# Kernel tuning notes

Measured on AMD Instinct MI355X. Metric: run time of the kernel, lower is better.

## Reference

```python
import jax, jax.numpy as jnp
import numpy as np

ATTN_WINDOW = 7  # attention_window from attn_params; dilation (attention_stride) = 1


def _xavier(key, shape):
    lim = np.sqrt(6.0 / (shape[0] + shape[1]))
    return jax.random.uniform(key, shape, jnp.float32, -lim, lim)


def setup_inputs() -> dict:
    key = jax.random.key(0)
    ks = jax.random.split(key, 8)
    B, Cin, Him, Wim = 4, 3, 112, 112
    Cmid, Cout = 128, 128
    x = jax.random.normal(ks[0], (B, Cin, Him, Wim), jnp.float32)
    conv_w = jax.random.normal(ks[1], (Cmid, Cin, 3, 3), jnp.float32) * 0.1  # OIHW
    conv_b = jnp.zeros((Cmid,), jnp.float32)
    q_w = _xavier(ks[2], (Cmid, Cmid)); q_b = jnp.zeros((Cmid,), jnp.float32)
    k_w = _xavier(ks[3], (Cmid, Cmid)); k_b = jnp.zeros((Cmid,), jnp.float32)
    v_w = _xavier(ks[4], (Cout, Cmid)); v_b = jnp.zeros((Cout,), jnp.float32)
    return {"x": x, "conv_w": conv_w, "conv_b": conv_b,
            "q_w": q_w, "q_b": q_b, "k_w": k_w, "k_b": k_b, "v_w": v_w, "v_b": v_b}


def _neighbor_idx(n, ksz):
    # NATTEN-style neighborhood: centered window, clamped to stay inside the image.
    starts = jnp.clip(jnp.arange(n) - ksz // 2, 0, n - ksz)
    return starts[:, None] + jnp.arange(ksz)[None, :]  # [n, ksz]


def reference(x, conv_w, conv_b, q_w, q_b, k_w, k_b, v_w, v_b):
    # conv stem (3x3, stride 2, pad 1) + ReLU
    f = jax.lax.conv_general_dilated(
        x, conv_w, window_strides=(2, 2), padding=[(1, 1), (1, 1)],
        dimension_numbers=("NCHW", "OIHW", "NCHW"))
    f = jax.nn.relu(f + conv_b[None, :, None, None])
    f = f.transpose(0, 2, 3, 1)  # NHWC  [B,H,W,Cmid]
    # 1x1 convs == per-pixel linear layers
    q = f @ q_w.T + q_b
    k = f @ k_w.T + k_b
    v = f @ v_w.T + v_b
    B, H, W, C = q.shape
    ksz = min(ATTN_WINDOW, H, W)
    ksz -= 1 if ksz % 2 == 0 else 0
    ih = _neighbor_idx(H, ksz)  # [H, ksz]
    iw = _neighbor_idx(W, ksz)  # [W, ksz]
    # gather per-pixel neighborhoods: [B,H,W,ksz,ksz,C]
    kn = k[:, ih[:, None, :, None], iw[None, :, None, :], :]
    vn = v[:, ih[:, None, :, None], iw[None, :, None, :], :]
    scale = C ** -0.5
    logits = jnp.einsum("bhwc,bhwijc->bhwij", q * scale, kn)
    attn = jax.nn.softmax(logits.reshape(B, H, W, -1), axis=-1).reshape(logits.shape)
    out = jnp.einsum("bhwij,bhwijc->bhwc", attn, vn)  # [B,H,W,Cout]
    return out.transpose(0, 3, 1, 2)  # back to NCHW
```

## Files before the change

kernel.cpp:

```cpp
#include <hip/hip_runtime.h>
#include <hip/hip_bf16.h>
#include <math.h>

#define HW 56
#define PPI (HW*HW)
#define NB 4
#define C 128
#define NPIX (NB*PPI)

typedef __attribute__((ext_vector_type(8))) short short8;
typedef __attribute__((ext_vector_type(4))) float f32x4;

__device__ __forceinline__ short bfbits(float v) {
    __hip_bfloat16 hb = __float2bfloat16(v);
    return *reinterpret_cast<short*>(&hb);
}

__global__ __launch_bounds__(256) void prep_kernel(
    const float* __restrict__ cw,
    const float* __restrict__ qw, const float* __restrict__ kw,
    const float* __restrict__ vw,
    __hip_bfloat16* __restrict__ wcf, __hip_bfloat16* __restrict__ wqkv)
{
    int gid = blockIdx.x * 256 + threadIdx.x;
    if (blockIdx.x < 192) {
        int m   = gid >> 14;
        int r   = gid & 16383;
        int col = r >> 7;
        int k   = r & 127;
        const float* W = (m == 0) ? qw : (m == 1) ? kw : vw;
        int kk = k >> 5, hi = (k >> 3) & 3, j = k & 7;
        wqkv[m * 16384 + ((kk * 4 + hi) * 128 + col) * 8 + j] = __float2bfloat16(W[col * 128 + k]);
    } else {
        int idx = gid - 192 * 256;
        int hi = idx >> 10, cout = (idx >> 3) & 127, j = idx & 7;
        int k  = hi * 8 + j;
        float v = (k < 27) ? cw[cout * 27 + k] : 0.f;
        wcf[(hi * 128 + cout) * 8 + j] = __float2bfloat16(v);
    }
}

__global__ __launch_bounds__(256) void convqkv_kernel(
    const float* __restrict__ x, const __hip_bfloat16* __restrict__ wcf,
    const float* __restrict__ cb, const __hip_bfloat16* __restrict__ wqkv,
    const float* __restrict__ qb, const float* __restrict__ kb,
    const float* __restrict__ vb,
    __hip_bfloat16* __restrict__ qo, __hip_bfloat16* __restrict__ ko,
    __hip_bfloat16* __restrict__ vo)
{
    __shared__ __align__(16) short f_lds[16 * 128];

    int t = threadIdx.x, lane = t & 63, wid = t >> 6;
    int r16 = lane & 15, hi = lane >> 4;

    int bx = blockIdx.x;
    int bimg = bx / 196;
    int rr = bx % 196;
    int th = rr / 14, tw = rr % 14;

    int h = th * 4 + (r16 >> 2), w = tw * 4 + (r16 & 3);
    short8 af;
    #pragma unroll
    for (int j = 0; j < 8; ++j) {
        int k = hi * 8 + j;
        float xv = 0.f;
        if (k < 27) {
            int ci = k / 9, r9 = k % 9;
            int kh = r9 / 3, kw_ = r9 % 3;
            int ih = 2 * h - 1 + kh, iw = 2 * w - 1 + kw_;
            if (ih >= 0 && ih < 112 && iw >= 0 && iw < 112)
                xv = x[((size_t)(bimg * 3 + ci) * 112 + ih) * 112 + iw];
        }
        af[j] = bfbits(xv);
    }

    #pragma unroll
    for (int ctl = 0; ctl < 2; ++ctl) {
        int ct = wid * 2 + ctl;
        int cout = ct * 16 + r16;
        short8 bw = *(const short8*)((const short*)wcf + (hi * 128 + cout) * 8);
        f32x4 acc = {0.f, 0.f, 0.f, 0.f};
        acc = __builtin_amdgcn_mfma_f32_16x16x32_bf16(af, bw, acc, 0, 0, 0);
        float bias = cb[cout];
        int colblk = cout >> 3, inb = (cout & 7) * 2;
        #pragma unroll
        for (int rg = 0; rg < 4; ++rg) {
            int px = hi * 4 + rg;
            float v = fmaxf(acc[rg] + bias, 0.f);
            *(short*)((char*)f_lds + px * 256 + ((colblk ^ px) << 4) + inb) = bfbits(v);
        }
    }
    __syncthreads();

    short8 fa[4];
    #pragma unroll
    for (int kk = 0; kk < 4; ++kk) {
        int colblk = kk * 4 + hi;
        fa[kk] = *(const short8*)((char*)f_lds + r16 * 256 + ((colblk ^ r16) << 4));
    }

    #pragma unroll
    for (int i = 0; i < 6; ++i) {
        int idx = wid * 6 + i;
        int mat = idx >> 3, nt = idx & 7;
        const short* wb = (const short*)wqkv + mat * 16384 + hi * 1024 + r16 * 8 + nt * 128;
        f32x4 acc = {0.f, 0.f, 0.f, 0.f};
        acc = __builtin_amdgcn_mfma_f32_16x16x32_bf16(fa[0], *(const short8*)(wb),         acc, 0, 0, 0);
        acc = __builtin_amdgcn_mfma_f32_16x16x32_bf16(fa[1], *(const short8*)(wb +  4096), acc, 0, 0, 0);
        acc = __builtin_amdgcn_mfma_f32_16x16x32_bf16(fa[2], *(const short8*)(wb +  8192), acc, 0, 0, 0);
        acc = __builtin_amdgcn_mfma_f32_16x16x32_bf16(fa[3], *(const short8*)(wb + 12288), acc, 0, 0, 0);
        int col = nt * 16 + r16;
        const float* Bv   = (mat == 0) ? qb : (mat == 1) ? kb : vb;
        __hip_bfloat16* O = (mat == 0) ? qo : (mat == 1) ? ko : vo;
        float bb = Bv[col];
        #pragma unroll
        for (int rg = 0; rg < 4; ++rg) {
            int px = hi * 4 + rg;
            int hh = th * 4 + (px >> 2), ww = tw * 4 + (px & 3);
            O[((size_t)(bimg * PPI + hh * HW + ww)) * C + col] = __float2bfloat16(acc[rg] + bb);
        }
    }
}

#define VPITCH 272

__global__ __launch_bounds__(256) void attn_kernel(
    const __hip_bfloat16* __restrict__ qg, const __hip_bfloat16* __restrict__ kg,
    const __hip_bfloat16* __restrict__ vg, float* __restrict__ out)
{
    __shared__ __align__(16) short vT[128 * 136];
    __shared__ __align__(16) float logit_s[16 * 116];
    __shared__ __align__(16) short attnW[16 * 136];

    int t    = threadIdx.x;
    int lane = t & 63, wid = t >> 6;
    int r16  = lane & 15, hi = lane >> 4;

    int bx = blockIdx.x;
    int b  = bx / 196;
    int rr = bx % 196;
    int th = rr / 14, tw = rr % 14;
    int ih0 = min(max(th*4 - 3, 0), HW - 10);
    int iw0 = min(max(tw*4 - 3, 0), HW - 10);

    {
        unsigned* aw = (unsigned*)attnW;
        for (int i = t; i < 1088; i += 256) aw[i] = 0u;
    }

    const unsigned* vgu = (const unsigned*)vg;
    #pragma unroll 4
    for (int it = 0; it < 16; ++it) {
        int i  = t + 256*it;
        int np = i >> 6;
        int c2 = i & 63;
        int n0 = min(2*np,     99);
        int n1 = min(2*np + 1, 99);
        int p0 = b*PPI + (ih0 + n0/10)*HW + (iw0 + n0%10);
        int p1 = b*PPI + (ih0 + n1/10)*HW + (iw0 + n1%10);
        unsigned av = vgu[(size_t)p0*64 + c2];
        unsigned bv = vgu[(size_t)p1*64 + c2];
        unsigned w0 = (av & 0xffffu) | (bv << 16);
        unsigned w1 = (av >> 16)     | (bv & 0xffff0000u);
        int c    = 2*c2;
        int hsw  = (c >> 3) & 7;
        int off  = (4*np) ^ (hsw << 4);
        *(unsigned*)((char*)vT + c*VPITCH + off)          = w0;
        *(unsigned*)((char*)vT + c*VPITCH + VPITCH + off) = w1;
    }

    int ph = th*4 + (r16 >> 2), pw = tw*4 + (r16 & 3);
    const short* qrow = (const short*)qg + (size_t)(b*PPI + ph*HW + pw)*C + hi*8;
    short8 qa0 = *(const short8*)(qrow);
    short8 qa1 = *(const short8*)(qrow + 32);
    short8 qa2 = *(const short8*)(qrow + 64);
    short8 qa3 = *(const short8*)(qrow + 96);

    __syncthreads();

    for (int nt = wid; nt < 7; nt += 4) {
        int n  = nt*16 + r16;
        int nc = min(n, 99);
        int kp = b*PPI + (ih0 + nc/10)*HW + (iw0 + nc%10);
        const short* krow = (const short*)kg + (size_t)kp*C + hi*8;
        f32x4 acc = {0.f, 0.f, 0.f, 0.f};
        acc = __builtin_amdgcn_mfma_f32_16x16x32_bf16(qa0, *(const short8*)(krow),      acc, 0, 0, 0);
        acc = __builtin_amdgcn_mfma_f32_16x16x32_bf16(qa1, *(const short8*)(krow + 32), acc, 0, 0, 0);
        acc = __builtin_amdgcn_mfma_f32_16x16x32_bf16(qa2, *(const short8*)(krow + 64), acc, 0, 0, 0);
        acc = __builtin_amdgcn_mfma_f32_16x16x32_bf16(qa3, *(const short8*)(krow + 96), acc, 0, 0, 0);
        #pragma unroll
        for (int rg = 0; rg < 4; ++rg)
            logit_s[(hi*4 + rg)*116 + nt*16 + r16] = acc[rg];
    }
    __syncthreads();

    {
        int r7 = lane / 7, s7 = lane - 7*r7;
        bool valid = lane < 49;
        const float scale = 0.08838834764831845f;
        #pragma unroll
        for (int px = 0; px < 4; ++px) {
            int p = wid*4 + px;
            int h = th*4 + (p >> 2), w = tw*4 + (p & 3);
            int hs = min(max(h - 3, 0), HW - 7);
            int ws = min(max(w - 3, 0), HW - 7);
            int col = (hs - ih0 + r7)*10 + (ws - iw0 + s7);
            float lg = valid ? logit_s[p*116 + col] * scale : -INFINITY;
            float m = lg;
            #pragma unroll
            for (int d = 1; d < 64; d <<= 1) m = fmaxf(m, __shfl_xor(m, d));
            float e = valid ? __expf(lg - m) : 0.f;
            float s = e;
            #pragma unroll
            for (int d = 1; d < 64; d <<= 1) s += __shfl_xor(s, d);
            if (valid) {
                __hip_bfloat16 hb = __float2bfloat16(e / s);
                *(__hip_bfloat16*)((char*)attnW + p*VPITCH + 2*col) = hb;
            }
        }
    }
    __syncthreads();

    short8 pa[4];
    #pragma unroll
    for (int kk = 0; kk < 4; ++kk)
        pa[kk] = *(const short8*)((char*)attnW + r16*VPITCH + kk*64 + hi*16);

    for (int nt = wid; nt < 8; nt += 4) {
        int c   = nt*16 + r16;
        int hsw = (c >> 3) & 7;
        const char* vrow = (const char*)vT + c*VPITCH;
        f32x4 acc = {0.f, 0.f, 0.f, 0.f};
        #pragma unroll
        for (int kk = 0; kk < 4; ++kk) {
            short8 vb = *(const short8*)(vrow + ((kk*64 + hi*16) ^ (hsw << 4)));
            acc = __builtin_amdgcn_mfma_f32_16x16x32_bf16(pa[kk], vb, acc, 0, 0, 0);
        }
        #pragma unroll
        for (int rg = 0; rg < 4; ++rg) {
            int p = hi*4 + rg;
            int h = th*4 + (p >> 2), w = tw*4 + (p & 3);
            out[(((size_t)b*C + c)*HW + h)*HW + w] = acc[rg];
        }
    }
}

extern "C" void kernel_launch(void* const* d_in, const int* in_sizes, int n_in,
                              void* d_out, int out_size, void* d_ws, size_t ws_size,
                              hipStream_t stream) {
    const float* x      = (const float*)d_in[0];
    const float* conv_w = (const float*)d_in[1];
    const float* conv_b = (const float*)d_in[2];
    const float* q_w    = (const float*)d_in[3];
    const float* q_b    = (const float*)d_in[4];
    const float* k_w    = (const float*)d_in[5];
    const float* k_b    = (const float*)d_in[6];
    const float* v_w    = (const float*)d_in[7];
    const float* v_b    = (const float*)d_in[8];
    float* out = (float*)d_out;

    __hip_bfloat16* q_bf  = (__hip_bfloat16*)d_ws;
    __hip_bfloat16* k_bf  = q_bf + (size_t)NPIX * C;
    __hip_bfloat16* v_bf  = k_bf + (size_t)NPIX * C;
    __hip_bfloat16* wqkv  = v_bf + (size_t)NPIX * C;
    __hip_bfloat16* wcf   = wqkv + 3 * 16384;

    prep_kernel<<<208, 256, 0, stream>>>(conv_w, q_w, k_w, v_w, wcf, wqkv);
    convqkv_kernel<<<NB*196, 256, 0, stream>>>(x, wcf, conv_b, wqkv,
                                               q_b, k_b, v_b, q_bf, k_bf, v_bf);
    attn_kernel<<<NB*196, 256, 0, stream>>>(q_bf, k_bf, v_bf, out);
}
```

Measured before the change: 44.44 us.

## Fuse conv stem, QKV projection and neighborhood attention into one kernel

Replaces the separate conv+QKV kernel and attention kernel with a single fused kernel. Each block recomputes the conv stem and K/V projections for its 10x10 neighborhood halo directly into LDS, and computes Q only for its own 16 pixels. This removes the bf16 Q/K/V workspace writes and reads and one launch, but redundantly recomputes halo features and raises LDS usage, which limits occupancy.

```diff
diff --git a/kernel.cpp b/kernel.cpp
--- a/kernel.cpp
+++ b/kernel.cpp
@@ -14,6 +14,9 @@
 __device__ __forceinline__ short bfbits(float v) {
     __hip_bfloat16 hb = __float2bfloat16(v);
     return *reinterpret_cast<short*>(&hb);
+}
+__device__ __forceinline__ unsigned packbf(float a, float b) {
+    return (unsigned)(unsigned short)bfbits(a) | ((unsigned)(unsigned short)bfbits(b) << 16);
 }
 
 __global__ __launch_bounds__(256) void prep_kernel(
@@ -40,101 +43,24 @@
     }
 }
 
-__global__ __launch_bounds__(256) void convqkv_kernel(
+#define VPITCH 272
+
+__global__ __launch_bounds__(256, 2) void fused_kernel(
     const float* __restrict__ x, const __hip_bfloat16* __restrict__ wcf,
     const float* __restrict__ cb, const __hip_bfloat16* __restrict__ wqkv,
     const float* __restrict__ qb, const float* __restrict__ kb,
-    const float* __restrict__ vb,
-    __hip_bfloat16* __restrict__ qo, __hip_bfloat16* __restrict__ ko,
-    __hip_bfloat16* __restrict__ vo)
+    const float* __restrict__ vb, float* __restrict__ out)
 {
-    __shared__ __align__(16) short f_lds[16 * 128];
+    __shared__ __align__(16) short k_lds[112 * 128];
+    __shared__ __align__(16) short vT[128 * 136];
+    __shared__ __align__(16) short q_lds[16 * 128];
+    __shared__ __align__(16) char  uni_s[16 * 116 * 4];
+    __shared__ __align__(16) short attnW[16 * 136];
+    short* f_ch    = (short*)uni_s;
+    float* logit_s = (float*)uni_s;
 
     int t = threadIdx.x, lane = t & 63, wid = t >> 6;
     int r16 = lane & 15, hi = lane >> 4;
-
-    int bx = blockIdx.x;
-    int bimg = bx / 196;
-    int rr = bx % 196;
-    int th = rr / 14, tw = rr % 14;
-
-    int h = th * 4 + (r16 >> 2), w = tw * 4 + (r16 & 3);
-    short8 af;
-    #pragma unroll
-    for (int j = 0; j < 8; ++j) {
-        int k = hi * 8 + j;
-        float xv = 0.f;
-        if (k < 27) {
-            int ci = k / 9, r9 = k % 9;
-            int kh = r9 / 3, kw_ = r9 % 3;
-            int ih = 2 * h - 1 + kh, iw = 2 * w - 1 + kw_;
-            if (ih >= 0 && ih < 112 && iw >= 0 && iw < 112)
-                xv = x[((size_t)(bimg * 3 + ci) * 112 + ih) * 112 + iw];
-        }
-        af[j] = bfbits(xv);
-    }
-
-    #pragma unroll
-    for (int ctl = 0; ctl < 2; ++ctl) {
-        int ct = wid * 2 + ctl;
-        int cout = ct * 16 + r16;
-        short8 bw = *(const short8*)((const short*)wcf + (hi * 128 + cout) * 8);
-        f32x4 acc = {0.f, 0.f, 0.f, 0.f};
-        acc = __builtin_amdgcn_mfma_f32_16x16x32_bf16(af, bw, acc, 0, 0, 0);
-        float bias = cb[cout];
-        int colblk = cout >> 3, inb = (cout & 7) * 2;
-        #pragma unroll
-        for (int rg = 0; rg < 4; ++rg) {
-            int px = hi * 4 + rg;
-            float v = fmaxf(acc[rg] + bias, 0.f);
-            *(short*)((char*)f_lds + px * 256 + ((colblk ^ px) << 4) + inb) = bfbits(v);
-        }
-    }
-    __syncthreads();
-
-    short8 fa[4];
-    #pragma unroll
-    for (int kk = 0; kk < 4; ++kk) {
-        int colblk = kk * 4 + hi;
-        fa[kk] = *(const short8*)((char*)f_lds + r16 * 256 + ((colblk ^ r16) << 4));
-    }
-
-    #pragma unroll
-    for (int i = 0; i < 6; ++i) {
-        int idx = wid * 6 + i;
-        int mat = idx >> 3, nt = idx & 7;
-        const short* wb = (const short*)wqkv + mat * 16384 + hi * 1024 + r16 * 8 + nt * 128;
-        f32x4 acc = {0.f, 0.f, 0.f, 0.f};
-        acc = __builtin_amdgcn_mfma_f32_16x16x32_bf16(fa[0], *(const short8*)(wb),         acc, 0, 0, 0);
-        acc = __builtin_amdgcn_mfma_f32_16x16x32_bf16(fa[1], *(const short8*)(wb +  4096), acc, 0, 0, 0);
-        acc = __builtin_amdgcn_mfma_f32_16x16x32_bf16(fa[2], *(const short8*)(wb +  8192), acc, 0, 0, 0);
-        acc = __builtin_amdgcn_mfma_f32_16x16x32_bf16(fa[3], *(const short8*)(wb + 12288), acc, 0, 0, 0);
-        int col = nt * 16 + r16;
-        const float* Bv   = (mat == 0) ? qb : (mat == 1) ? kb : vb;
-        __hip_bfloat16* O = (mat == 0) ? qo : (mat == 1) ? ko : vo;
-        float bb = Bv[col];
-        #pragma unroll
-        for (int rg = 0; rg < 4; ++rg) {
-            int px = hi * 4 + rg;
-            int hh = th * 4 + (px >> 2), ww = tw * 4 + (px & 3);
-            O[((size_t)(bimg * PPI + hh * HW + ww)) * C + col] = __float2bfloat16(acc[rg] + bb);
-        }
-    }
-}
-
-#define VPITCH 272
-
-__global__ __launch_bounds__(256) void attn_kernel(
-    const __hip_bfloat16* __restrict__ qg, const __hip_bfloat16* __restrict__ kg,
-    const __hip_bfloat16* __restrict__ vg, float* __restrict__ out)
-{
-    __shared__ __align__(16) short vT[128 * 136];
-    __shared__ __align__(16) float logit_s[16 * 116];
-    __shared__ __align__(16) short attnW[16 * 136];
-
-    int t    = threadIdx.x;
-    int lane = t & 63, wid = t >> 6;
-    int r16  = lane & 15, hi = lane >> 4;
 
     int bx = blockIdx.x;
     int b  = bx / 196;
@@ -146,48 +72,138 @@
     {
         unsigned* aw = (unsigned*)attnW;
         for (int i = t; i < 1088; i += 256) aw[i] = 0u;
-    }
-
-    const unsigned* vgu = (const unsigned*)vg;
-    #pragma unroll 4
-    for (int it = 0; it < 16; ++it) {
-        int i  = t + 256*it;
-        int np = i >> 6;
-        int c2 = i & 63;
-        int n0 = min(2*np,     99);
-        int n1 = min(2*np + 1, 99);
-        int p0 = b*PPI + (ih0 + n0/10)*HW + (iw0 + n0%10);
-        int p1 = b*PPI + (ih0 + n1/10)*HW + (iw0 + n1%10);
-        unsigned av = vgu[(size_t)p0*64 + c2];
-        unsigned bv = vgu[(size_t)p1*64 + c2];
-        unsigned w0 = (av & 0xffffu) | (bv << 16);
-        unsigned w1 = (av >> 16)     | (bv & 0xffff0000u);
-        int c    = 2*c2;
-        int hsw  = (c >> 3) & 7;
-        int off  = (4*np) ^ (hsw << 4);
-        *(unsigned*)((char*)vT + c*VPITCH + off)          = w0;
-        *(unsigned*)((char*)vT + c*VPITCH + VPITCH + off) = w1;
-    }
-
-    int ph = th*4 + (r16 >> 2), pw = tw*4 + (r16 & 3);
-    const short* qrow = (const short*)qg + (size_t)(b*PPI + ph*HW + pw)*C + hi*8;
-    short8 qa0 = *(const short8*)(qrow);
-    short8 qa1 = *(const short8*)(qrow + 32);
-    short8 qa2 = *(const short8*)(qrow + 64);
-    short8 qa3 = *(const short8*)(qrow + 96);
-
-    __syncthreads();
+        for (int i = t; i < 1024; i += 256) {
+            int c = i >> 3, j = i & 7;
+            int hsw = (c >> 3) & 7;
+            int unit = (14 + (j >> 2)) ^ hsw;
+            *(unsigned*)((char*)vT + c*VPITCH + (unit << 4) + (j & 3)*4) = 0u;
+        }
+    }
+
+    int cout0 = (wid*2 + 0)*16 + r16;
+    int cout1 = (wid*2 + 1)*16 + r16;
+    short8 cbw0 = *(const short8*)((const short*)wcf + (hi*128 + cout0)*8);
+    short8 cbw1 = *(const short8*)((const short*)wcf + (hi*128 + cout1)*8);
+
+    auto conv_to_fch = [&](int hf, int wf) {
+        short8 af;
+        #pragma unroll
+        for (int j = 0; j < 8; ++j) {
+            int k = hi*8 + j;
+            float xv = 0.f;
+            if (k < 27) {
+                int ci = k/9, r9 = k%9, kh = r9/3, kw_ = r9%3;
+                int ih = 2*hf - 1 + kh, iw = 2*wf - 1 + kw_;
+                if (ih >= 0 && ih < 112 && iw >= 0 && iw < 112)
+                    xv = x[((size_t)(b*3 + ci)*112 + ih)*112 + iw];
+            }
+            af[j] = bfbits(xv);
+        }
+        #pragma unroll
+        for (int ctl = 0; ctl < 2; ++ctl) {
+            int cout  = ctl ? cout1 : cout0;
+            short8 bw = ctl ? cbw1  : cbw0;
+            f32x4 acc = {0.f, 0.f, 0.f, 0.f};
+            acc = __builtin_amdgcn_mfma_f32_16x16x32_bf16(af, bw, acc, 0, 0, 0);
+            float bias = cb[cout];
+            int colblk = cout >> 3, inb = (cout & 7)*2;
+            #pragma unroll
+            for (int rg = 0; rg < 4; ++rg) {
+                int px = hi*4 + rg;
+                *(short*)((char*)f_ch + px*256 + ((colblk ^ px) << 4) + inb)
+                    = bfbits(fmaxf(acc[rg] + bias, 0.f));
+            }
+        }
+    };
+
+    for (int cc = 0; cc < 7; ++cc) {
+        int nc = min(cc*16 + r16, 99);
+        conv_to_fch(ih0 + nc/10, iw0 + nc%10);
+        __syncthreads();
+
+        short8 fa[4];
+        #pragma unroll
+        for (int kk = 0; kk < 4; ++kk)
+            fa[kk] = *(const short8*)((char*)f_ch + r16*256 + (((kk*4 + hi) ^ r16) << 4));
+
+        #pragma unroll
+        for (int i = 0; i < 4; ++i) {
+            int idx = wid*4 + i;
+            int mv  = idx >> 3;
+            int ct  = idx & 7;
+            const short* wb = (const short*)wqkv + (1+mv)*16384 + hi*1024 + r16*8 + ct*128;
+            f32x4 acc = {0.f, 0.f, 0.f, 0.f};
+            acc = __builtin_amdgcn_mfma_f32_16x16x32_bf16(fa[0], *(const short8*)(wb),         acc, 0, 0, 0);
+            acc = __builtin_amdgcn_mfma_f32_16x16x32_bf16(fa[1], *(const short8*)(wb +  4096), acc, 0, 0, 0);
+            acc = __builtin_amdgcn_mfma_f32_16x16x32_bf16(fa[2], *(const short8*)(wb +  8192), acc, 0, 0, 0);
+            acc = __builtin_amdgcn_mfma_f32_16x16x32_bf16(fa[3], *(const short8*)(wb + 12288), acc, 0, 0, 0);
+            int c = ct*16 + r16;
+            if (mv == 0) {
+                float bb = kb[c];
+                int swz = c >> 3;
+                #pragma unroll
+                for (int rg = 0; rg < 4; ++rg) {
+                    int n = cc*16 + hi*4 + rg;
+                    *(short*)((char*)k_lds + n*256 + ((swz ^ (n & 15)) << 4) + (c & 7)*2)
+                        = bfbits(acc[rg] + bb);
+                }
+            } else {
+                float bb = vb[c];
+                int n0 = cc*16 + hi*4;
+                unsigned lo  = packbf(acc[0] + bb, acc[1] + bb);
+                unsigned hi2 = packbf(acc[2] + bb, acc[3] + bb);
+                int hsw = (c >> 3) & 7;
+                int off = (2*n0) ^ (hsw << 4);
+                *(uint2*)((char*)vT + c*VPITCH + off) = make_uint2(lo, hi2);
+            }
+        }
+        __syncthreads();
+    }
+
+    {
+        int ph = th*4 + (r16 >> 2), pw = tw*4 + (r16 & 3);
+        conv_to_fch(ph, pw);
+        __syncthreads();
+
+        short8 fa[4];
+        #pragma unroll
+        for (int kk = 0; kk < 4; ++kk)
+            fa[kk] = *(const short8*)((char*)f_ch + r16*256 + (((kk*4 + hi) ^ r16) << 4));
+
+        #pragma unroll
+        for (int i = 0; i < 2; ++i) {
+            int ct = wid*2 + i;
+            const short* wb = (const short*)wqkv + hi*1024 + r16*8 + ct*128;
+            f32x4 acc = {0.f, 0.f, 0.f, 0.f};
+            acc = __builtin_amdgcn_mfma_f32_16x16x32_bf16(fa[0], *(const short8*)(wb),         acc, 0, 0, 0);
+            acc = __builtin_amdgcn_mfma_f32_16x16x32_bf16(fa[1], *(const short8*)(wb +  4096), acc, 0, 0, 0);
+            acc = __builtin_amdgcn_mfma_f32_16x16x32_bf16(fa[2], *(const short8*)(wb +  8192), acc, 0, 0, 0);
+            acc = __builtin_amdgcn_mfma_f32_16x16x32_bf16(fa[3], *(const short8*)(wb + 12288), acc, 0, 0, 0);
+            int c = ct*16 + r16;
+            float bb = qb[c];
+            #pragma unroll
+            for (int rg = 0; rg < 4; ++rg) {
+                int px = hi*4 + rg;
+                *(short*)((char*)q_lds + px*256 + (((c >> 3) ^ px) << 4) + (c & 7)*2)
+                    = bfbits(acc[rg] + bb);
+            }
+        }
+        __syncthreads();
+    }
+
+    short8 qa[4];
+    #pragma unroll
+    for (int kk = 0; kk < 4; ++kk)
+        qa[kk] = *(const short8*)((char*)q_lds + r16*256 + (((kk*4 + hi) ^ r16) << 4));
 
     for (int nt = wid; nt < 7; nt += 4) {
-        int n  = nt*16 + r16;
-        int nc = min(n, 99);
-        int kp = b*PPI + (ih0 + nc/10)*HW + (iw0 + nc%10);
-        const short* krow = (const short*)kg + (size_t)kp*C + hi*8;
+        const char* kb_ = (const char*)k_lds + (nt*16 + r16)*256;
         f32x4 acc = {0.f, 0.f, 0.f, 0.f};
-        acc = __builtin_amdgcn_mfma_f32_16x16x32_bf16(qa0, *(const short8*)(krow),      acc, 0, 0, 0);
-        acc = __builtin_amdgcn_mfma_f32_16x16x32_bf16(qa1, *(const short8*)(krow + 32), acc, 0, 0, 0);
-        acc = __builtin_amdgcn_mfma_f32_16x16x32_bf16(qa2, *(const short8*)(krow + 64), acc, 0, 0, 0);
-        acc = __builtin_amdgcn_mfma_f32_16x16x32_bf16(qa3, *(const short8*)(krow + 96), acc, 0, 0, 0);
+        #pragma unroll
+        for (int kk = 0; kk < 4; ++kk) {
+            short8 kv = *(const short8*)(kb_ + (((kk*4 + hi) ^ r16) << 4));
+            acc = __builtin_amdgcn_mfma_f32_16x16x32_bf16(qa[kk], kv, acc, 0, 0, 0);
+        }
         #pragma unroll
         for (int rg = 0; rg < 4; ++rg)
             logit_s[(hi*4 + rg)*116 + nt*16 + r16] = acc[rg];
@@ -233,8 +249,8 @@
         f32x4 acc = {0.f, 0.f, 0.f, 0.f};
         #pragma unroll
         for (int kk = 0; kk < 4; ++kk) {
-            short8 vb = *(const short8*)(vrow + ((kk*64 + hi*16) ^ (hsw << 4)));
-            acc = __builtin_amdgcn_mfma_f32_16x16x32_bf16(pa[kk], vb, acc, 0, 0, 0);
+            short8 vbr = *(const short8*)(vrow + ((kk*64 + hi*16) ^ (hsw << 4)));
+            acc = __builtin_amdgcn_mfma_f32_16x16x32_bf16(pa[kk], vbr, acc, 0, 0, 0);
         }
         #pragma unroll
         for (int rg = 0; rg < 4; ++rg) {
@@ -259,14 +275,10 @@
     const float* v_b    = (const float*)d_in[8];
     float* out = (float*)d_out;
 
-    __hip_bfloat16* q_bf  = (__hip_bfloat16*)d_ws;
-    __hip_bfloat16* k_bf  = q_bf + (size_t)NPIX * C;
-    __hip_bfloat16* v_bf  = k_bf + (size_t)NPIX * C;
-    __hip_bfloat16* wqkv  = v_bf + (size_t)NPIX * C;
-    __hip_bfloat16* wcf   = wqkv + 3 * 16384;
+    __hip_bfloat16* wqkv = (__hip_bfloat16*)d_ws;
+    __hip_bfloat16* wcf  = wqkv + 3 * 16384;
 
     prep_kernel<<<208, 256, 0, stream>>>(conv_w, q_w, k_w, v_w, wcf, wqkv);
-    convqkv_kernel<<<NB*196, 256, 0, stream>>>(x, wcf, conv_b, wqkv,
-                                               q_b, k_b, v_b, q_bf, k_bf, v_bf);
-    attn_kernel<<<NB*196, 256, 0, stream>>>(q_bf, k_bf, v_bf, out);
-}
+    fused_kernel<<<NB*196, 256, 0, stream>>>(x, wcf, conv_b, wqkv,
+                                             q_b, k_b, v_b, out);
+}
```

Result: slower. 62.53 us (+40.7%).
